# Performance work log

Measured on AMD Instinct MI355X. Metric: run time of the kernel, lower is better.

Reference implementation:

```python
import jax, jax.numpy as jnp
import numpy as np

B, L, E, D1, D2 = 256, 128, 64, 512, 512


def setup_inputs() -> dict:
    key = jax.random.key(0)
    k1, k2, k3, kw = jax.random.split(key, 4)
    tensor1 = jax.random.normal(k1, (B, L, D1), dtype=jnp.float32)
    tensor2 = jax.random.normal(k2, (B, L, D2), dtype=jnp.float32)
    parameters_index = jax.random.randint(k3, (B,), 0, E, dtype=jnp.int32)
    # xavier_uniform with relu gain: gain*sqrt(6/(fan_in+fan_out)),
    # torch fan for [E,D1,D2]: fan_in = D1*D2, fan_out = E*D2
    gain = float(np.sqrt(2.0))
    bound = gain * float(np.sqrt(6.0 / (D1 * D2 + E * D2)))
    weights = jax.random.uniform(kw, (E, D1, D2), minval=-bound, maxval=bound, dtype=jnp.float32)
    return {"tensor1": tensor1, "tensor2": tensor2, "parameters_index": parameters_index, "weights": weights}


def reference(tensor1, tensor2, parameters_index, weights):
    # gather per-batch weight matrix [B, D1, D2], then bilinear form x1^T W x2
    w = weights[parameters_index]  # [B, D1, D2]
    # equals: sum over i,j of tensor1[b,l,i] * w[b,i,j] * tensor2[b,l,j] -> [B, L]
    return jnp.einsum('bli,bij,blj->bl', tensor1, w, tensor2)
```

## Files before the change

### kernel.cpp

```cpp
#include <hip/hip_runtime.h>
#include <stdint.h>

#define NB 256
#define NL 128
#define ND1 512
#define ND2 512

#define BI 64
#define NIT (ND1 / BI)
#define NKT (ND2 / 32)

typedef float float4_t __attribute__((ext_vector_type(4)));
typedef __bf16 bf16x8_t __attribute__((ext_vector_type(8)));
typedef unsigned short ushort8_t __attribute__((ext_vector_type(8)));

__device__ __forceinline__ unsigned short f2bf(float f) {
    unsigned int u = __float_as_uint(f);
    u += 0x7FFFu + ((u >> 16) & 1u);
    return (unsigned short)(u >> 16);
}

__device__ __forceinline__ ushort8_t pack8(float4_t lo, float4_t hi) {
    ushort8_t u;
    u[0] = f2bf(lo.x); u[1] = f2bf(lo.y); u[2] = f2bf(lo.z); u[3] = f2bf(lo.w);
    u[4] = f2bf(hi.x); u[5] = f2bf(hi.y); u[6] = f2bf(hi.z); u[7] = f2bf(hi.w);
    return u;
}

__global__ __launch_bounds__(1024, 4) void pdot_kernel(
    const float* __restrict__ t1, const float* __restrict__ t2,
    const int* __restrict__ pidx, const float* __restrict__ wgt,
    float* __restrict__ out)
{
    __shared__ unsigned short sW[2][BI * ND2];

    const int b  = blockIdx.x;
    const int t  = threadIdx.x;
    const int wv = t >> 6;
    const int mg = wv >> 1;
    const int ng = wv & 1;
    const int ln = t & 63;
    const int nh = ln & 15;
    const int qd = ln >> 4;

    const int e = pidx[b];
    const float* wp  = wgt + (size_t)e * (ND1 * ND2);
    const float* t1p = t1  + (size_t)b * (NL * ND1);

    const int sr  = t >> 4;
    const int sc  = t & 15;
    const int ssw = sr & 31;

    const int lrow = mg * 16 + nh;
    const float* aRow = t2 + (size_t)b * (NL * ND2) + (size_t)lrow * ND2 + qd * 8;
    bf16x8_t afrag[NKT];
    #pragma unroll
    for (int kt = 0; kt < NKT; ++kt) {
        float4_t lo = *(const float4_t*)(aRow + kt * 32);
        float4_t hi = *(const float4_t*)(aRow + kt * 32 + 4);
        afrag[kt] = __builtin_bit_cast(bf16x8_t, pack8(lo, hi));
    }

    {
        const float* src = wp + (size_t)sr * ND2;
        unsigned short* dst = &sW[0][sr * ND2];
        #pragma unroll
        for (int q = 0; q < 4; ++q) {
            const int c = sc + 16 * q;
            float4_t lo = *(const float4_t*)(src + c * 8);
            float4_t hi = *(const float4_t*)(src + c * 8 + 4);
            *(ushort8_t*)(dst + (c ^ ssw) * 8) = pack8(lo, hi);
        }
    }
    __syncthreads();

    const int r0 = ng * 32 + nh;
    const int r1 = ng * 32 + 16 + nh;
    const unsigned short* wb0base;
    const int sw0 = r0 & 31;
    const int sw1 = r1 & 31;

    float4_t ps = {0.f, 0.f, 0.f, 0.f};

    for (int it = 0; it < NIT; ++it) {
        const int cur = it & 1;

        if (it < NIT - 1) {
            const float* src = wp + (size_t)((it + 1) * BI + sr) * ND2;
            unsigned short* dst = &sW[cur ^ 1][sr * ND2];
            #pragma unroll
            for (int q = 0; q < 4; ++q) {
                const int c = sc + 16 * q;
                float4_t lo = *(const float4_t*)(src + c * 8);
                float4_t hi = *(const float4_t*)(src + c * 8 + 4);
                *(ushort8_t*)(dst + (c ^ ssw) * 8) = pack8(lo, hi);
            }
        }

        float4_t acc0 = {0.f, 0.f, 0.f, 0.f};
        float4_t acc1 = {0.f, 0.f, 0.f, 0.f};
        const unsigned short* sb = &sW[cur][0];
        #pragma unroll
        for (int kt = 0; kt < NKT; ++kt) {
            const int c = kt * 4 + qd;
            bf16x8_t b0 = __builtin_bit_cast(bf16x8_t,
                *(const ushort8_t*)(sb + r0 * ND2 + (c ^ sw0) * 8));
            acc0 = __builtin_amdgcn_mfma_f32_16x16x32_bf16(afrag[kt], b0, acc0, 0, 0, 0);
            bf16x8_t b1 = __builtin_bit_cast(bf16x8_t,
                *(const ushort8_t*)(sb + r1 * ND2 + (c ^ sw1) * 8));
            acc1 = __builtin_amdgcn_mfma_f32_16x16x32_bf16(afrag[kt], b1, acc1, 0, 0, 0);
        }

        const int colbase = it * BI + ng * 32;
        #pragma unroll
        for (int r = 0; r < 4; ++r) {
            const int row = mg * 16 + qd * 4 + r;
            ps[r] += acc0[r] * t1p[(size_t)row * ND1 + colbase + nh]
                   + acc1[r] * t1p[(size_t)row * ND1 + colbase + 16 + nh];
        }

        __syncthreads();
    }
    (void)wb0base;

    #pragma unroll
    for (int r = 0; r < 4; ++r) {
        float v = ps[r];
        v += __shfl_xor(v, 1);
        v += __shfl_xor(v, 2);
        v += __shfl_xor(v, 4);
        v += __shfl_xor(v, 8);
        if (nh == 0) atomicAdd(&out[b * NL + mg * 16 + qd * 4 + r], v);
    }
}

extern "C" void kernel_launch(void* const* d_in, const int* in_sizes, int n_in,
                              void* d_out, int out_size, void* d_ws, size_t ws_size,
                              hipStream_t stream)
{
    const float* t1  = (const float*)d_in[0];
    const float* t2  = (const float*)d_in[1];
    const int* pidx  = (const int*)d_in[2];
    const float* wgt = (const float*)d_in[3];
    float* out = (float*)d_out;

    hipMemsetAsync(out, 0, (size_t)out_size * sizeof(float), stream);
    pdot_kernel<<<dim3(NB), dim3(1024), 0, stream>>>(t1, t2, pidx, wgt, out);
}
```

Measured before the change: 251.9 us.

## Use single 128-row weight slab and stream t2 fragments per slab

```diff
diff --git a/kernel.cpp b/kernel.cpp
--- a/kernel.cpp
+++ b/kernel.cpp
@@ -6,8 +6,8 @@
 #define ND1 512
 #define ND2 512
 
-#define BI 64
-#define NIT (ND1 / BI)
+#define BI 128
+#define NSL (ND1 / BI)
 #define NKT (ND2 / 32)
 
 typedef float float4_t __attribute__((ext_vector_type(4)));
@@ -32,13 +32,13 @@
     const int* __restrict__ pidx, const float* __restrict__ wgt,
     float* __restrict__ out)
 {
-    __shared__ unsigned short sW[2][BI * ND2];
+    __shared__ unsigned short sW[BI * ND2];
 
     const int b  = blockIdx.x;
     const int t  = threadIdx.x;
     const int wv = t >> 6;
     const int mg = wv >> 1;
-    const int ng = wv & 1;
+    const int ih = wv & 1;
     const int ln = t & 63;
     const int nh = ln & 15;
     const int qd = ln >> 4;
@@ -46,82 +46,83 @@
     const int e = pidx[b];
     const float* wp  = wgt + (size_t)e * (ND1 * ND2);
     const float* t1p = t1  + (size_t)b * (NL * ND1);
+    const float* aRow = t2 + (size_t)b * (NL * ND2) + (size_t)(mg * 16 + nh) * ND2 + qd * 8;
 
-    const int sr  = t >> 4;
-    const int sc  = t & 15;
+    const int sr  = t >> 3;
+    const int sc  = t & 7;
     const int ssw = sr & 31;
+    unsigned short* dstrow = &sW[sr * ND2];
 
-    const int lrow = mg * 16 + nh;
-    const float* aRow = t2 + (size_t)b * (NL * ND2) + (size_t)lrow * ND2 + qd * 8;
-    bf16x8_t afrag[NKT];
+    int rrow[4], rsw[4];
     #pragma unroll
-    for (int kt = 0; kt < NKT; ++kt) {
-        float4_t lo = *(const float4_t*)(aRow + kt * 32);
-        float4_t hi = *(const float4_t*)(aRow + kt * 32 + 4);
-        afrag[kt] = __builtin_bit_cast(bf16x8_t, pack8(lo, hi));
+    for (int ns = 0; ns < 4; ++ns) {
+        rrow[ns] = ih * 64 + ns * 16 + nh;
+        rsw[ns]  = rrow[ns] & 31;
     }
-
-    {
-        const float* src = wp + (size_t)sr * ND2;
-        unsigned short* dst = &sW[0][sr * ND2];
-        #pragma unroll
-        for (int q = 0; q < 4; ++q) {
-            const int c = sc + 16 * q;
-            float4_t lo = *(const float4_t*)(src + c * 8);
-            float4_t hi = *(const float4_t*)(src + c * 8 + 4);
-            *(ushort8_t*)(dst + (c ^ ssw) * 8) = pack8(lo, hi);
-        }
-    }
-    __syncthreads();
-
-    const int r0 = ng * 32 + nh;
-    const int r1 = ng * 32 + 16 + nh;
-    const unsigned short* wb0base;
-    const int sw0 = r0 & 31;
-    const int sw1 = r1 & 31;
 
     float4_t ps = {0.f, 0.f, 0.f, 0.f};
 
-    for (int it = 0; it < NIT; ++it) {
-        const int cur = it & 1;
+    for (int s = 0; s < NSL; ++s) {
+        if (s > 0) __syncthreads();
 
-        if (it < NIT - 1) {
-            const float* src = wp + (size_t)((it + 1) * BI + sr) * ND2;
-            unsigned short* dst = &sW[cur ^ 1][sr * ND2];
+        {
+            const float* src = wp + (size_t)(s * BI + sr) * ND2;
             #pragma unroll
-            for (int q = 0; q < 4; ++q) {
-                const int c = sc + 16 * q;
-                float4_t lo = *(const float4_t*)(src + c * 8);
-                float4_t hi = *(const float4_t*)(src + c * 8 + 4);
-                *(ushort8_t*)(dst + (c ^ ssw) * 8) = pack8(lo, hi);
+            for (int h = 0; h < 2; ++h) {
+                float4_t wl[4][2];
+                #pragma unroll
+                for (int q = 0; q < 4; ++q) {
+                    const int c = sc + 8 * (h * 4 + q);
+                    wl[q][0] = *(const float4_t*)(src + c * 8);
+                    wl[q][1] = *(const float4_t*)(src + c * 8 + 4);
+                }
+                #pragma unroll
+                for (int q = 0; q < 4; ++q) {
+                    const int c = sc + 8 * (h * 4 + q);
+                    *(ushort8_t*)(dstrow + ((c ^ ssw) * 8)) = pack8(wl[q][0], wl[q][1]);
+                }
             }
         }
 
-        float4_t acc0 = {0.f, 0.f, 0.f, 0.f};
-        float4_t acc1 = {0.f, 0.f, 0.f, 0.f};
-        const unsigned short* sb = &sW[cur][0];
+        float4_t ra[4][2];
+        #pragma unroll
+        for (int p = 0; p < 4; ++p) {
+            ra[p][0] = *(const float4_t*)(aRow + p * 32);
+            ra[p][1] = *(const float4_t*)(aRow + p * 32 + 4);
+        }
+
+        __syncthreads();
+
+        float4_t acc[4];
+        #pragma unroll
+        for (int ns = 0; ns < 4; ++ns) { float4_t z = {0.f,0.f,0.f,0.f}; acc[ns] = z; }
+
         #pragma unroll
         for (int kt = 0; kt < NKT; ++kt) {
-            const int c = kt * 4 + qd;
-            bf16x8_t b0 = __builtin_bit_cast(bf16x8_t,
-                *(const ushort8_t*)(sb + r0 * ND2 + (c ^ sw0) * 8));
-            acc0 = __builtin_amdgcn_mfma_f32_16x16x32_bf16(afrag[kt], b0, acc0, 0, 0, 0);
-            bf16x8_t b1 = __builtin_bit_cast(bf16x8_t,
-                *(const ushort8_t*)(sb + r1 * ND2 + (c ^ sw1) * 8));
-            acc1 = __builtin_amdgcn_mfma_f32_16x16x32_bf16(afrag[kt], b1, acc1, 0, 0, 0);
+            bf16x8_t af = __builtin_bit_cast(bf16x8_t, pack8(ra[kt & 3][0], ra[kt & 3][1]));
+            if (kt < NKT - 4) {
+                ra[kt & 3][0] = *(const float4_t*)(aRow + (kt + 4) * 32);
+                ra[kt & 3][1] = *(const float4_t*)(aRow + (kt + 4) * 32 + 4);
+            }
+            #pragma unroll
+            for (int ns = 0; ns < 4; ++ns) {
+                const int chunk = (kt * 4 + qd) ^ rsw[ns];
+                bf16x8_t bfr = __builtin_bit_cast(bf16x8_t,
+                    *(const ushort8_t*)(&sW[rrow[ns] * ND2 + chunk * 8]));
+                acc[ns] = __builtin_amdgcn_mfma_f32_16x16x32_bf16(af, bfr, acc[ns], 0, 0, 0);
+            }
         }
 
-        const int colbase = it * BI + ng * 32;
+        const int colbase = s * BI + ih * 64;
         #pragma unroll
         for (int r = 0; r < 4; ++r) {
             const int row = mg * 16 + qd * 4 + r;
-            ps[r] += acc0[r] * t1p[(size_t)row * ND1 + colbase + nh]
-                   + acc1[r] * t1p[(size_t)row * ND1 + colbase + 16 + nh];
+            const float* t1r = t1p + (size_t)row * ND1 + colbase + nh;
+            #pragma unroll
+            for (int ns = 0; ns < 4; ++ns)
+                ps[r] += acc[ns][r] * t1r[ns * 16];
         }
-
-        __syncthreads();
     }
-    (void)wb0base;
 
     #pragma unroll
     for (int r = 0; r < 4; ++r) {
```

Measured after the change: 295.5 us. 17.3% more time.
